# Optimization experiments

Hardware: AMD Instinct MI355X
Metric: run time of the kernel (lower is better)

Reference implementation:

```python
import jax, jax.numpy as jnp
import numpy as np

G = 60            # 60x60 macroblock MV grid (960px / 16px blocks)
IMAGE_SIZE = 960.0
LN_EPS = 1e-5


def layer_norm(x, g, b):
    mu = jnp.mean(x, -1, keepdims=True)
    var = jnp.var(x, -1, keepdims=True)
    return (x - mu) / jnp.sqrt(var + LN_EPS) * g + b


def setup_inputs() -> dict:
    key = jax.random.key(0)
    ks = iter(jax.random.split(key, 40))
    nk = lambda: next(ks)
    N = 4096
    MVF, BED, H = 64, 32, 128
    D_IN = MVF + BED  # 96

    def lin(out_d, in_d):
        w = jax.random.normal(nk(), (out_d, in_d), jnp.float32) * np.float32(1.0 / np.sqrt(in_d))
        b = jnp.zeros((out_d,), jnp.float32)
        return w, b

    motion_vectors = jax.random.normal(nk(), (1, 2, G, G), jnp.float32)
    xy = jax.random.uniform(nk(), (N, 2), jnp.float32, 0.0, 800.0)
    wh = jax.random.uniform(nk(), (N, 2), jnp.float32, 16.0, 160.0)
    boxes = jnp.concatenate([xy, jnp.clip(xy + wh, 0.0, IMAGE_SIZE)], axis=-1)

    inp = {"motion_vectors": motion_vectors, "boxes": boxes}
    # stats projection: 6 stats (mean/std/range x 2 channels) -> MVF
    inp["W_stats"], inp["b_stats"] = lin(MVF, 6)
    inp["g_stats"] = jnp.ones((MVF,), jnp.float32); inp["be_stats"] = jnp.zeros((MVF,), jnp.float32)
    # box coordinate encoder
    inp["W_b1"], inp["b_b1"] = lin(BED, 4)
    inp["g_b1"] = jnp.ones((BED,), jnp.float32); inp["be_b1"] = jnp.zeros((BED,), jnp.float32)
    inp["W_b2"], inp["b_b2"] = lin(BED, BED)
    inp["g_b2"] = jnp.ones((BED,), jnp.float32); inp["be_b2"] = jnp.zeros((BED,), jnp.float32)
    # single-layer LSTM (torch gate order i,f,g,o)
    inp["W_ih"] = jax.random.normal(nk(), (4 * H, D_IN), jnp.float32) * np.float32(1.0 / np.sqrt(D_IN))
    inp["W_hh"] = jax.random.normal(nk(), (4 * H, H), jnp.float32) * np.float32(1.0 / np.sqrt(H))
    inp["b_ih"] = jnp.zeros((4 * H,), jnp.float32)
    inp["b_hh"] = jnp.zeros((4 * H,), jnp.float32)
    # heads
    inp["W_p1"], inp["b_p1"] = lin(H // 2, H); inp["W_p2"], inp["b_p2"] = lin(2, H // 2)
    inp["W_s1"], inp["b_s1"] = lin(H // 2, H); inp["W_s2"], inp["b_s2"] = lin(2, H // 2)
    inp["W_c1"], inp["b_c1"] = lin(H // 2, H); inp["W_c2"], inp["b_c2"] = lin(1, H // 2)
    return inp


def _box_motion_stats(motion_vectors, boxes_norm):
    # motion_vectors: [1,2,G,G]; boxes_norm: [N,4] in [0,1]
    mvf = motion_vectors[0].reshape(2, G * G)  # [2, 3600]
    x1 = jnp.clip(jnp.floor(boxes_norm[:, 0] * G).astype(jnp.int32), 0, G - 1)
    y1 = jnp.clip(jnp.floor(boxes_norm[:, 1] * G).astype(jnp.int32), 0, G - 1)
    x2 = jnp.clip(jnp.ceil(boxes_norm[:, 2] * G).astype(jnp.int32), x1 + 1, G)
    y2 = jnp.clip(jnp.ceil(boxes_norm[:, 3] * G).astype(jnp.int32), y1 + 1, G)
    idx = jnp.arange(G)
    mx = (idx[None, :] >= x1[:, None]) & (idx[None, :] < x2[:, None])  # [N,G]
    my = (idx[None, :] >= y1[:, None]) & (idx[None, :] < y2[:, None])  # [N,G]
    mask = (my[:, :, None] & mx[:, None, :]).reshape(-1, G * G).astype(mvf.dtype)  # [N,3600]
    cnt = mask.sum(-1, keepdims=True)  # >= 1 by construction
    s = jnp.einsum('nc,kc->nk', mask, mvf)          # [N,2]
    sq = jnp.einsum('nc,kc->nk', mask, mvf * mvf)   # [N,2]
    mean = s / cnt
    std = jnp.sqrt(jnp.clip(sq / cnt - mean * mean, 0.0))
    big = jnp.asarray(1e30, mvf.dtype)
    hi = jnp.where(mask[:, None, :] > 0, mvf[None], -big).max(-1)  # [N,2]
    lo = jnp.where(mask[:, None, :] > 0, mvf[None], big).min(-1)   # [N,2]
    return jnp.concatenate([mean, std, hi - lo], axis=-1)  # [N,6]


def reference(motion_vectors, boxes,
              W_stats, b_stats, g_stats, be_stats,
              W_b1, b_b1, g_b1, be_b1, W_b2, b_b2, g_b2, be_b2,
              W_ih, W_hh, b_ih, b_hh,
              W_p1, b_p1, W_p2, b_p2, W_s1, b_s1, W_s2, b_s2, W_c1, b_c1, W_c2, b_c2):
    N = boxes.shape[0]
    H = W_hh.shape[1]
    boxes_norm = jnp.clip(boxes / IMAGE_SIZE, 0.0, 1.0)

    # per-box motion feature (BoxAlignedMotionEncoder: gather region -> mean/std/range -> proj)
    stats = _box_motion_stats(motion_vectors, boxes_norm)
    mv_feat = jax.nn.relu(layer_norm(stats @ W_stats.T + b_stats, g_stats, be_stats))  # [N,64]

    # box coordinate encoder (dropout = identity in eval)
    h1 = jax.nn.relu(layer_norm(boxes_norm @ W_b1.T + b_b1, g_b1, be_b1))
    box_feat = jax.nn.relu(layer_norm(h1 @ W_b2.T + b_b2, g_b2, be_b2))  # [N,32]

    x = jnp.concatenate([mv_feat, box_feat], axis=-1)  # [N,96]

    # single-step LSTM, zero initial state, torch gate order i,f,g,o
    h0 = jnp.zeros((N, H), x.dtype)
    c0 = jnp.zeros((N, H), x.dtype)
    gates = x @ W_ih.T + h0 @ W_hh.T + b_ih + b_hh
    i, f, g, o = jnp.split(gates, 4, axis=-1)
    c = jax.nn.sigmoid(f) * c0 + jax.nn.sigmoid(i) * jnp.tanh(g)
    h = jax.nn.sigmoid(o) * jnp.tanh(c)  # [N,128]

    pos = jax.nn.relu(h @ W_p1.T + b_p1) @ W_p2.T + b_p2    # [N,2]
    size = jax.nn.relu(h @ W_s1.T + b_s1) @ W_s2.T + b_s2   # [N,2]
    conf = jax.nn.relu(h @ W_c1.T + b_c1) @ W_c2.T + b_c2   # [N,1]
    confidences = jax.nn.sigmoid(conf[:, 0])

    # box update: shift center by deltas, scale w/h by exp(size_deltas)
    x1, y1, x2, y2 = boxes[:, 0], boxes[:, 1], boxes[:, 2], boxes[:, 3]
    cx, cy = (x1 + x2) * 0.5, (y1 + y2) * 0.5
    w, hgt = x2 - x1, y2 - y1
    ncx, ncy = cx + pos[:, 0], cy + pos[:, 1]
    nw, nh = w * jnp.exp(size[:, 0]), hgt * jnp.exp(size[:, 1])
    pred = jnp.stack([ncx - nw * 0.5, ncy - nh * 0.5, ncx + nw * 0.5, ncy + nh * 0.5], axis=-1)
    return jnp.concatenate([pred, confidences[:, None]], axis=-1)  # [N,5]
```

## Files before the change

kernel.cpp:

```cpp
#include <hip/hip_runtime.h>
#include <math.h>

#define GRID_G 60
#define GRID_GG 3600
#define BPB 8

__device__ __forceinline__ float wred32sum(float v){
  #pragma unroll
  for (int m = 16; m; m >>= 1) v += __shfl_xor(v, m, 32);
  return v;
}
__device__ __forceinline__ float wred32max(float v){
  #pragma unroll
  for (int m = 16; m; m >>= 1) v = fmaxf(v, __shfl_xor(v, m, 32));
  return v;
}
__device__ __forceinline__ float wred32min(float v){
  #pragma unroll
  for (int m = 16; m; m >>= 1) v = fminf(v, __shfl_xor(v, m, 32));
  return v;
}
__device__ __forceinline__ float frcp(float x){ return __builtin_amdgcn_rcpf(x); }
__device__ __forceinline__ float fsig(float x){ return frcp(1.0f + __expf(-x)); }
__device__ __forceinline__ float ftanh(float x){ return 1.0f - 2.0f * frcp(1.0f + __expf(2.0f * x)); }

__global__ __launch_bounds__(256) void tracker_kernel(
    const float* __restrict__ mv,
    const float* __restrict__ boxes,
    const float* __restrict__ W_stats, const float* __restrict__ b_stats,
    const float* __restrict__ g_stats, const float* __restrict__ be_stats,
    const float* __restrict__ W_b1,  const float* __restrict__ b_b1,
    const float* __restrict__ g_b1,  const float* __restrict__ be_b1,
    const float* __restrict__ W_b2,  const float* __restrict__ b_b2,
    const float* __restrict__ g_b2,  const float* __restrict__ be_b2,
    const float* __restrict__ W_ih,  const float* __restrict__ b_ih,
    const float* __restrict__ b_hh,
    const float* __restrict__ W_p1,  const float* __restrict__ b_p1,
    const float* __restrict__ W_p2,  const float* __restrict__ b_p2,
    const float* __restrict__ W_s1,  const float* __restrict__ b_s1,
    const float* __restrict__ W_s2,  const float* __restrict__ b_s2,
    const float* __restrict__ W_c1,  const float* __restrict__ b_c1,
    const float* __restrict__ W_c2,  const float* __restrict__ b_c2,
    float* __restrict__ out, int N)
{
  __shared__ __align__(16) float x_lds[BPB][96];
  __shared__ __align__(16) float h_lds[BPB][128];
  __shared__ __align__(16) float h1_lds[BPB][32];
  __shared__ float u_lds[3*BPB][65];
  __shared__ float res_lds[BPB][5];

  const int tid  = threadIdx.x;
  const int base = blockIdx.x * BPB;

  {
    const int b   = tid >> 5;
    const int l32 = tid & 31;
    int gb = base + b; if (gb >= N) gb = N - 1;
    const float4 bx = ((const float4*)boxes)[gb];
    const float bn0 = fminf(fmaxf(bx.x * (1.0f/960.0f), 0.f), 1.f);
    const float bn1 = fminf(fmaxf(bx.y * (1.0f/960.0f), 0.f), 1.f);
    const float bn2 = fminf(fmaxf(bx.z * (1.0f/960.0f), 0.f), 1.f);
    const float bn3 = fminf(fmaxf(bx.w * (1.0f/960.0f), 0.f), 1.f);

    int x1 = (int)floorf(bn0 * 60.f); x1 = min(max(x1, 0), 59);
    int y1 = (int)floorf(bn1 * 60.f); y1 = min(max(y1, 0), 59);
    int x2 = (int)ceilf (bn2 * 60.f); x2 = min(max(x2, x1 + 1), 60);
    int y2 = (int)ceilf (bn3 * 60.f); y2 = min(max(y2, y1 + 1), 60);
    const int w = x2 - x1, hh = y2 - y1;
    const int cnt = w * hh;
    const float rw = 1.0f / (float)w;

    float s0=0.f, s1=0.f, q0=0.f, q1=0.f;
    float hi0=-1e30f, hi1=-1e30f, lo0=1e30f, lo1=1e30f;
    for (int c = l32; c < cnt; c += 32) {
      const int yy = (int)(((float)c + 0.5f) * rw);
      const int xx = c - yy * w;
      const int idx = (y1 + yy) * GRID_G + (x1 + xx);
      const float m0 = mv[idx];
      const float m1 = mv[GRID_GG + idx];
      s0 += m0; q0 += m0*m0; hi0 = fmaxf(hi0, m0); lo0 = fminf(lo0, m0);
      s1 += m1; q1 += m1*m1; hi1 = fmaxf(hi1, m1); lo1 = fminf(lo1, m1);
    }
    s0 = wred32sum(s0); q0 = wred32sum(q0); hi0 = wred32max(hi0); lo0 = wred32min(lo0);
    s1 = wred32sum(s1); q1 = wred32sum(q1); hi1 = wred32max(hi1); lo1 = wred32min(lo1);
    const float inv = frcp((float)cnt);
    float st[6];
    st[0] = s0 * inv;
    st[1] = s1 * inv;
    st[2] = sqrtf(fmaxf(q0 * inv - st[0]*st[0], 0.f));
    st[3] = sqrtf(fmaxf(q1 * inv - st[1]*st[1], 0.f));
    st[4] = hi0 - lo0;
    st[5] = hi1 - lo1;

    {
      const float* Wr0 = W_stats + l32 * 6;
      const float* Wr1 = W_stats + (l32 + 32) * 6;
      float v0 = b_stats[l32];
      float v1 = b_stats[l32 + 32];
      #pragma unroll
      for (int k = 0; k < 6; ++k) { v0 += st[k] * Wr0[k]; v1 += st[k] * Wr1[k]; }
      const float mu  = wred32sum(v0 + v1) * (1.0f/64.0f);
      const float var = wred32sum(v0*v0 + v1*v1) * (1.0f/64.0f) - mu*mu;
      const float rs  = rsqrtf(var + 1e-5f);
      x_lds[b][l32     ] = fmaxf((v0 - mu) * rs * g_stats[l32     ] + be_stats[l32     ], 0.f);
      x_lds[b][l32 + 32] = fmaxf((v1 - mu) * rs * g_stats[l32 + 32] + be_stats[l32 + 32], 0.f);
    }

    {
      const float* Wr = W_b1 + l32 * 4;
      const float v = b_b1[l32] + bn0*Wr[0] + bn1*Wr[1] + bn2*Wr[2] + bn3*Wr[3];
      const float mu  = wred32sum(v)   * (1.0f/32.0f);
      const float var = wred32sum(v*v) * (1.0f/32.0f) - mu*mu;
      const float h1v = fmaxf((v - mu) * rsqrtf(var + 1e-5f) * g_b1[l32] + be_b1[l32], 0.f);
      h1_lds[b][l32] = h1v;
    }
    __threadfence_block();

    {
      const float* Wr = W_b2 + l32 * 32;
      float v = b_b2[l32];
      #pragma unroll
      for (int kk = 0; kk < 8; ++kk) {
        const float4 hv = *(const float4*)(&h1_lds[b][kk * 4]);
        const float4 wv = *(const float4*)(&Wr[kk * 4]);
        v = fmaf(wv.x,hv.x, fmaf(wv.y,hv.y, fmaf(wv.z,hv.z, fmaf(wv.w,hv.w, v))));
      }
      const float mu  = wred32sum(v)   * (1.0f/32.0f);
      const float var = wred32sum(v*v) * (1.0f/32.0f) - mu*mu;
      const float y = fmaxf((v - mu) * rsqrtf(var + 1e-5f) * g_b2[l32] + be_b2[l32], 0.f);
      x_lds[b][64 + l32] = y;
    }
  }
  __syncthreads();

  {
    const int j  = tid & 127;
    const int b0 = (tid >> 7) * 4;
    float ai[4] = {0,0,0,0}, ag[4] = {0,0,0,0}, ao[4] = {0,0,0,0};
    const float4* Wi = (const float4*)(W_ih + (size_t)(j      ) * 96);
    const float4* Wg = (const float4*)(W_ih + (size_t)(j + 256) * 96);
    const float4* Wo = (const float4*)(W_ih + (size_t)(j + 384) * 96);
    #pragma unroll 4
    for (int kk = 0; kk < 24; ++kk) {
      const float4 wi = Wi[kk], wg = Wg[kk], wo = Wo[kk];
      #pragma unroll
      for (int b = 0; b < 4; ++b) {
        const float4 xv = *(const float4*)(&x_lds[b0 + b][kk * 4]);
        ai[b] = fmaf(wi.x,xv.x, fmaf(wi.y,xv.y, fmaf(wi.z,xv.z, fmaf(wi.w,xv.w, ai[b]))));
        ag[b] = fmaf(wg.x,xv.x, fmaf(wg.y,xv.y, fmaf(wg.z,xv.z, fmaf(wg.w,xv.w, ag[b]))));
        ao[b] = fmaf(wo.x,xv.x, fmaf(wo.y,xv.y, fmaf(wo.z,xv.z, fmaf(wo.w,xv.w, ao[b]))));
      }
    }
    const float bi = b_ih[j      ] + b_hh[j      ];
    const float bg = b_ih[j + 256] + b_hh[j + 256];
    const float bo = b_ih[j + 384] + b_hh[j + 384];
    #pragma unroll
    for (int b = 0; b < 4; ++b) {
      const float c = fsig(ai[b] + bi) * ftanh(ag[b] + bg);
      h_lds[b0 + b][j] = fsig(ao[b] + bo) * ftanh(c);
    }
  }
  __syncthreads();

  if (tid < 192) {
    const int head = tid >> 6;
    const int l    = tid & 63;
    const float* W1 = (head == 0) ? W_p1 : (head == 1) ? W_s1 : W_c1;
    const float* B1 = (head == 0) ? b_p1 : (head == 1) ? b_s1 : b_c1;
    float acc[BPB] = {0,0,0,0,0,0,0,0};
    const float4* Wr = (const float4*)(W1 + (size_t)l * 128);
    #pragma unroll 4
    for (int kk = 0; kk < 32; ++kk) {
      const float4 w = Wr[kk];
      #pragma unroll
      for (int b = 0; b < BPB; ++b) {
        const float4 hv = *(const float4*)(&h_lds[b][kk * 4]);
        acc[b] = fmaf(w.x,hv.x, fmaf(w.y,hv.y, fmaf(w.z,hv.z, fmaf(w.w,hv.w, acc[b]))));
      }
    }
    const float bias = B1[l];
    #pragma unroll
    for (int b = 0; b < BPB; ++b)
      u_lds[head * BPB + b][l] = fmaxf(acc[b] + bias, 0.f);
  }
  __syncthreads();

  if (tid < BPB * 5) {
    const int b = tid / 5, o = tid % 5;
    const int head = (o < 2) ? 0 : (o < 4) ? 1 : 2;
    const float* W2; float bias;
    if      (o == 0) { W2 = W_p2;      bias = b_p2[0]; }
    else if (o == 1) { W2 = W_p2 + 64; bias = b_p2[1]; }
    else if (o == 2) { W2 = W_s2;      bias = b_s2[0]; }
    else if (o == 3) { W2 = W_s2 + 64; bias = b_s2[1]; }
    else             { W2 = W_c2;      bias = b_c2[0]; }
    const float* ur = u_lds[head * BPB + b];
    float a0 = bias, a1 = 0.f, a2 = 0.f, a3 = 0.f;
    #pragma unroll 4
    for (int k = 0; k < 64; k += 4) {
      a0 = fmaf(ur[k  ], W2[k  ], a0);
      a1 = fmaf(ur[k+1], W2[k+1], a1);
      a2 = fmaf(ur[k+2], W2[k+2], a2);
      a3 = fmaf(ur[k+3], W2[k+3], a3);
    }
    res_lds[b][o] = (a0 + a1) + (a2 + a3);
  }
  __syncthreads();

  if (tid < BPB) {
    const int gb = base + tid;
    if (gb < N) {
      const float4 bx = ((const float4*)boxes)[gb];
      const float cx = (bx.x + bx.z) * 0.5f;
      const float cy = (bx.y + bx.w) * 0.5f;
      const float w  = bx.z - bx.x;
      const float hh = bx.w - bx.y;
      const float ncx = cx + res_lds[tid][0];
      const float ncy = cy + res_lds[tid][1];
      const float nw  = w  * __expf(res_lds[tid][2]);
      const float nh  = hh * __expf(res_lds[tid][3]);
      const float cf  = fsig(res_lds[tid][4]);
      float* op = out + (size_t)gb * 5;
      op[0] = ncx - nw * 0.5f;
      op[1] = ncy - nh * 0.5f;
      op[2] = ncx + nw * 0.5f;
      op[3] = ncy + nh * 0.5f;
      op[4] = cf;
    }
  }
}

extern "C" void kernel_launch(void* const* d_in, const int* in_sizes, int n_in,
                              void* d_out, int out_size, void* d_ws, size_t ws_size,
                              hipStream_t stream) {
  (void)n_in; (void)out_size; (void)d_ws; (void)ws_size;
  const float* mv       = (const float*)d_in[0];
  const float* boxes    = (const float*)d_in[1];
  const float* W_stats  = (const float*)d_in[2];
  const float* b_stats  = (const float*)d_in[3];
  const float* g_stats  = (const float*)d_in[4];
  const float* be_stats = (const float*)d_in[5];
  const float* W_b1     = (const float*)d_in[6];
  const float* b_b1     = (const float*)d_in[7];
  const float* g_b1     = (const float*)d_in[8];
  const float* be_b1    = (const float*)d_in[9];
  const float* W_b2     = (const float*)d_in[10];
  const float* b_b2     = (const float*)d_in[11];
  const float* g_b2     = (const float*)d_in[12];
  const float* be_b2    = (const float*)d_in[13];
  const float* W_ih     = (const float*)d_in[14];
  const float* b_ih     = (const float*)d_in[16];
  const float* b_hh     = (const float*)d_in[17];
  const float* W_p1     = (const float*)d_in[18];
  const float* b_p1     = (const float*)d_in[19];
  const float* W_p2     = (const float*)d_in[20];
  const float* b_p2     = (const float*)d_in[21];
  const float* W_s1     = (const float*)d_in[22];
  const float* b_s1     = (const float*)d_in[23];
  const float* W_s2     = (const float*)d_in[24];
  const float* b_s2     = (const float*)d_in[25];
  const float* W_c1     = (const float*)d_in[26];
  const float* b_c1     = (const float*)d_in[27];
  const float* W_c2     = (const float*)d_in[28];
  const float* b_c2     = (const float*)d_in[29];

  const int N = in_sizes[1] / 4;
  const int grid = (N + BPB - 1) / BPB;
  tracker_kernel<<<grid, 256, 0, stream>>>(
      mv, boxes,
      W_stats, b_stats, g_stats, be_stats,
      W_b1, b_b1, g_b1, be_b1,
      W_b2, b_b2, g_b2, be_b2,
      W_ih, b_ih, b_hh,
      W_p1, b_p1, W_p2, b_p2,
      W_s1, b_s1, W_s2, b_s2,
      W_c1, b_c1, W_c2, b_c2,
      (float*)d_out, N);
}
```

Measured before the change: 151.6 us.

## Restructure tracker kernel to single-wavefront blocks of four boxes with DPP reductions

Switches from 256-thread blocks handling 8 boxes to 64-thread (one wavefront) blocks handling 4 boxes, with 16 lanes per box in the stats stage. Cross-lane reductions now use DPP and ds_swizzle/readlane instead of shfl, the box-encoder hidden vector is broadcast via ds_bpermute instead of LDS, and the head layers plus the final output are computed in registers, removing two barriers and two LDS buffers. In exchange each lane does more work per block and weights are re-read by twice as many blocks, raising total L2 weight traffic.

```diff
diff --git a/kernel.cpp b/kernel.cpp
--- a/kernel.cpp
+++ b/kernel.cpp
@@ -3,28 +3,43 @@
 
 #define GRID_G 60
 #define GRID_GG 3600
-#define BPB 8
-
-__device__ __forceinline__ float wred32sum(float v){
-  #pragma unroll
-  for (int m = 16; m; m >>= 1) v += __shfl_xor(v, m, 32);
+
+__device__ __forceinline__ int   f2i(float x){ return __float_as_int(x); }
+__device__ __forceinline__ float i2f(int x){ return __int_as_float(x); }
+
+template<int CTRL>
+__device__ __forceinline__ float dppmov(float v){
+  return i2f(__builtin_amdgcn_update_dpp(0, f2i(v), CTRL, 0xF, 0xF, true));
+}
+__device__ __forceinline__ float red16sum(float v){
+  v += dppmov<0xB1>(v); v += dppmov<0x4E>(v);
+  v += dppmov<0x124>(v); v += dppmov<0x128>(v);
   return v;
 }
-__device__ __forceinline__ float wred32max(float v){
-  #pragma unroll
-  for (int m = 16; m; m >>= 1) v = fmaxf(v, __shfl_xor(v, m, 32));
+__device__ __forceinline__ float red16max(float v){
+  v = fmaxf(v, dppmov<0xB1>(v));  v = fmaxf(v, dppmov<0x4E>(v));
+  v = fmaxf(v, dppmov<0x124>(v)); v = fmaxf(v, dppmov<0x128>(v));
   return v;
 }
-__device__ __forceinline__ float wred32min(float v){
-  #pragma unroll
-  for (int m = 16; m; m >>= 1) v = fminf(v, __shfl_xor(v, m, 32));
+__device__ __forceinline__ float red16min(float v){
+  v = fminf(v, dppmov<0xB1>(v));  v = fminf(v, dppmov<0x4E>(v));
+  v = fminf(v, dppmov<0x124>(v)); v = fminf(v, dppmov<0x128>(v));
   return v;
+}
+__device__ __forceinline__ float swz_xor16(float v){
+  return i2f(__builtin_amdgcn_ds_swizzle(f2i(v), 0x401F));
+}
+__device__ __forceinline__ float rdl(float v, int l){
+  return i2f(__builtin_amdgcn_readlane(f2i(v), l));
+}
+__device__ __forceinline__ float bperm(int idxbytes, float v){
+  return i2f(__builtin_amdgcn_ds_bpermute(idxbytes, f2i(v)));
 }
 __device__ __forceinline__ float frcp(float x){ return __builtin_amdgcn_rcpf(x); }
 __device__ __forceinline__ float fsig(float x){ return frcp(1.0f + __expf(-x)); }
-__device__ __forceinline__ float ftanh(float x){ return 1.0f - 2.0f * frcp(1.0f + __expf(2.0f * x)); }
-
-__global__ __launch_bounds__(256) void tracker_kernel(
+__device__ __forceinline__ float ftanh(float x){ return 1.0f - 2.0f*frcp(1.0f + __expf(2.0f*x)); }
+
+__global__ __launch_bounds__(64) void tracker_kernel(
     const float* __restrict__ mv,
     const float* __restrict__ boxes,
     const float* __restrict__ W_stats, const float* __restrict__ b_stats,
@@ -43,19 +58,16 @@
     const float* __restrict__ W_c2,  const float* __restrict__ b_c2,
     float* __restrict__ out, int N)
 {
-  __shared__ __align__(16) float x_lds[BPB][96];
-  __shared__ __align__(16) float h_lds[BPB][128];
-  __shared__ __align__(16) float h1_lds[BPB][32];
-  __shared__ float u_lds[3*BPB][65];
-  __shared__ float res_lds[BPB][5];
-
-  const int tid  = threadIdx.x;
-  const int base = blockIdx.x * BPB;
-
-  {
-    const int b   = tid >> 5;
-    const int l32 = tid & 31;
-    int gb = base + b; if (gb >= N) gb = N - 1;
+  __shared__ __align__(16) float x_lds[4][104];
+  __shared__ __align__(16) float h_lds[4][128];
+
+  const int lane = threadIdx.x;
+  const int grp  = lane >> 4;
+  const int l16  = lane & 15;
+  const int base = blockIdx.x * 4;
+
+  {
+    int gb = base + grp; if (gb >= N) gb = N - 1;
     const float4 bx = ((const float4*)boxes)[gb];
     const float bn0 = fminf(fmaxf(bx.x * (1.0f/960.0f), 0.f), 1.f);
     const float bn1 = fminf(fmaxf(bx.y * (1.0f/960.0f), 0.f), 1.f);
@@ -72,7 +84,7 @@
 
     float s0=0.f, s1=0.f, q0=0.f, q1=0.f;
     float hi0=-1e30f, hi1=-1e30f, lo0=1e30f, lo1=1e30f;
-    for (int c = l32; c < cnt; c += 32) {
+    for (int c = l16; c < cnt; c += 16) {
       const int yy = (int)(((float)c + 0.5f) * rw);
       const int xx = c - yy * w;
       const int idx = (y1 + yy) * GRID_G + (x1 + xx);
@@ -81,8 +93,8 @@
       s0 += m0; q0 += m0*m0; hi0 = fmaxf(hi0, m0); lo0 = fminf(lo0, m0);
       s1 += m1; q1 += m1*m1; hi1 = fmaxf(hi1, m1); lo1 = fminf(lo1, m1);
     }
-    s0 = wred32sum(s0); q0 = wred32sum(q0); hi0 = wred32max(hi0); lo0 = wred32min(lo0);
-    s1 = wred32sum(s1); q1 = wred32sum(q1); hi1 = wred32max(hi1); lo1 = wred32min(lo1);
+    s0 = red16sum(s0); q0 = red16sum(q0); hi0 = red16max(hi0); lo0 = red16min(lo0);
+    s1 = red16sum(s1); q1 = red16sum(q1); hi1 = red16max(hi1); lo1 = red16min(lo1);
     const float inv = frcp((float)cnt);
     float st[6];
     st[0] = s0 * inv;
@@ -93,139 +105,201 @@
     st[5] = hi1 - lo1;
 
     {
-      const float* Wr0 = W_stats + l32 * 6;
-      const float* Wr1 = W_stats + (l32 + 32) * 6;
-      float v0 = b_stats[l32];
-      float v1 = b_stats[l32 + 32];
-      #pragma unroll
-      for (int k = 0; k < 6; ++k) { v0 += st[k] * Wr0[k]; v1 += st[k] * Wr1[k]; }
-      const float mu  = wred32sum(v0 + v1) * (1.0f/64.0f);
-      const float var = wred32sum(v0*v0 + v1*v1) * (1.0f/64.0f) - mu*mu;
+      float vm[4], vsum = 0.f, vsq = 0.f;
+      #pragma unroll
+      for (int m = 0; m < 4; ++m) {
+        const int row = l16 + 16*m;
+        const float* Wr = W_stats + row * 6;
+        float v = b_stats[row];
+        #pragma unroll
+        for (int k = 0; k < 6; ++k) v = fmaf(st[k], Wr[k], v);
+        vm[m] = v; vsum += v; vsq = fmaf(v, v, vsq);
+      }
+      const float mu  = red16sum(vsum) * (1.0f/64.0f);
+      const float var = red16sum(vsq)  * (1.0f/64.0f) - mu*mu;
       const float rs  = rsqrtf(var + 1e-5f);
-      x_lds[b][l32     ] = fmaxf((v0 - mu) * rs * g_stats[l32     ] + be_stats[l32     ], 0.f);
-      x_lds[b][l32 + 32] = fmaxf((v1 - mu) * rs * g_stats[l32 + 32] + be_stats[l32 + 32], 0.f);
-    }
-
+      #pragma unroll
+      for (int m = 0; m < 4; ++m) {
+        const int row = l16 + 16*m;
+        x_lds[grp][row] = fmaxf((vm[m]-mu)*rs*g_stats[row] + be_stats[row], 0.f);
+      }
+    }
+
+    float h1a, h1b;
     {
-      const float* Wr = W_b1 + l32 * 4;
-      const float v = b_b1[l32] + bn0*Wr[0] + bn1*Wr[1] + bn2*Wr[2] + bn3*Wr[3];
-      const float mu  = wred32sum(v)   * (1.0f/32.0f);
-      const float var = wred32sum(v*v) * (1.0f/32.0f) - mu*mu;
-      const float h1v = fmaxf((v - mu) * rsqrtf(var + 1e-5f) * g_b1[l32] + be_b1[l32], 0.f);
-      h1_lds[b][l32] = h1v;
-    }
-    __threadfence_block();
+      const float* Wa = W_b1 + l16 * 4;
+      const float* Wb = W_b1 + (l16 + 16) * 4;
+      const float v0 = b_b1[l16]    + bn0*Wa[0] + bn1*Wa[1] + bn2*Wa[2] + bn3*Wa[3];
+      const float v1 = b_b1[l16+16] + bn0*Wb[0] + bn1*Wb[1] + bn2*Wb[2] + bn3*Wb[3];
+      const float mu  = red16sum(v0 + v1) * (1.0f/32.0f);
+      const float var = red16sum(v0*v0 + v1*v1) * (1.0f/32.0f) - mu*mu;
+      const float rs  = rsqrtf(var + 1e-5f);
+      h1a = fmaxf((v0-mu)*rs*g_b1[l16]    + be_b1[l16],    0.f);
+      h1b = fmaxf((v1-mu)*rs*g_b1[l16+16] + be_b1[l16+16], 0.f);
+    }
 
     {
-      const float* Wr = W_b2 + l32 * 32;
-      float v = b_b2[l32];
-      #pragma unroll
-      for (int kk = 0; kk < 8; ++kk) {
-        const float4 hv = *(const float4*)(&h1_lds[b][kk * 4]);
-        const float4 wv = *(const float4*)(&Wr[kk * 4]);
-        v = fmaf(wv.x,hv.x, fmaf(wv.y,hv.y, fmaf(wv.z,hv.z, fmaf(wv.w,hv.w, v))));
-      }
-      const float mu  = wred32sum(v)   * (1.0f/32.0f);
-      const float var = wred32sum(v*v) * (1.0f/32.0f) - mu*mu;
-      const float y = fmaxf((v - mu) * rsqrtf(var + 1e-5f) * g_b2[l32] + be_b2[l32], 0.f);
-      x_lds[b][64 + l32] = y;
+      const int gbyte = (lane & 48) << 2;
+      const float* Wa = W_b2 + l16 * 32;
+      const float* Wb = W_b2 + (l16 + 16) * 32;
+      float u0 = b_b2[l16], u1 = b_b2[l16+16];
+      #pragma unroll
+      for (int k = 0; k < 16; ++k) {
+        const float hk = bperm(gbyte + (k << 2), h1a);
+        u0 = fmaf(Wa[k], hk, u0); u1 = fmaf(Wb[k], hk, u1);
+      }
+      #pragma unroll
+      for (int k = 0; k < 16; ++k) {
+        const float hk = bperm(gbyte + (k << 2), h1b);
+        u0 = fmaf(Wa[16+k], hk, u0); u1 = fmaf(Wb[16+k], hk, u1);
+      }
+      const float mu  = red16sum(u0 + u1) * (1.0f/32.0f);
+      const float var = red16sum(u0*u0 + u1*u1) * (1.0f/32.0f) - mu*mu;
+      const float rs  = rsqrtf(var + 1e-5f);
+      x_lds[grp][64 + l16] = fmaxf((u0-mu)*rs*g_b2[l16]    + be_b2[l16],    0.f);
+      x_lds[grp][80 + l16] = fmaxf((u1-mu)*rs*g_b2[l16+16] + be_b2[l16+16], 0.f);
     }
   }
   __syncthreads();
 
-  {
-    const int j  = tid & 127;
-    const int b0 = (tid >> 7) * 4;
-    float ai[4] = {0,0,0,0}, ag[4] = {0,0,0,0}, ao[4] = {0,0,0,0};
-    const float4* Wi = (const float4*)(W_ih + (size_t)(j      ) * 96);
-    const float4* Wg = (const float4*)(W_ih + (size_t)(j + 256) * 96);
-    const float4* Wo = (const float4*)(W_ih + (size_t)(j + 384) * 96);
-    #pragma unroll 4
+  float hA[4], hB[4];
+  {
+    const float4* Wi0 = (const float4*)(W_ih + (size_t)(lane      ) * 96);
+    const float4* Wi1 = (const float4*)(W_ih + (size_t)(lane +  64) * 96);
+    const float4* Wg0 = (const float4*)(W_ih + (size_t)(lane + 256) * 96);
+    const float4* Wg1 = (const float4*)(W_ih + (size_t)(lane + 320) * 96);
+    const float4* Wo0 = (const float4*)(W_ih + (size_t)(lane + 384) * 96);
+    const float4* Wo1 = (const float4*)(W_ih + (size_t)(lane + 448) * 96);
+    float aI0[4]={0,0,0,0}, aI1[4]={0,0,0,0};
+    float aG0[4]={0,0,0,0}, aG1[4]={0,0,0,0};
+    float aO0[4]={0,0,0,0}, aO1[4]={0,0,0,0};
+    #pragma unroll 2
     for (int kk = 0; kk < 24; ++kk) {
-      const float4 wi = Wi[kk], wg = Wg[kk], wo = Wo[kk];
+      const float4 wi0 = Wi0[kk], wi1 = Wi1[kk];
+      const float4 wg0 = Wg0[kk], wg1 = Wg1[kk];
+      const float4 wo0 = Wo0[kk], wo1 = Wo1[kk];
+      float4 xv[4];
+      #pragma unroll
+      for (int b = 0; b < 4; ++b) xv[b] = *(const float4*)(&x_lds[b][kk*4]);
       #pragma unroll
       for (int b = 0; b < 4; ++b) {
-        const float4 xv = *(const float4*)(&x_lds[b0 + b][kk * 4]);
-        ai[b] = fmaf(wi.x,xv.x, fmaf(wi.y,xv.y, fmaf(wi.z,xv.z, fmaf(wi.w,xv.w, ai[b]))));
-        ag[b] = fmaf(wg.x,xv.x, fmaf(wg.y,xv.y, fmaf(wg.z,xv.z, fmaf(wg.w,xv.w, ag[b]))));
-        ao[b] = fmaf(wo.x,xv.x, fmaf(wo.y,xv.y, fmaf(wo.z,xv.z, fmaf(wo.w,xv.w, ao[b]))));
-      }
-    }
-    const float bi = b_ih[j      ] + b_hh[j      ];
-    const float bg = b_ih[j + 256] + b_hh[j + 256];
-    const float bo = b_ih[j + 384] + b_hh[j + 384];
-    #pragma unroll
-    for (int b = 0; b < 4; ++b) {
-      const float c = fsig(ai[b] + bi) * ftanh(ag[b] + bg);
-      h_lds[b0 + b][j] = fsig(ao[b] + bo) * ftanh(c);
+        const float4 x4 = xv[b];
+        aI0[b] = fmaf(wi0.x,x4.x, fmaf(wi0.y,x4.y, fmaf(wi0.z,x4.z, fmaf(wi0.w,x4.w, aI0[b]))));
+        aI1[b] = fmaf(wi1.x,x4.x, fmaf(wi1.y,x4.y, fmaf(wi1.z,x4.z, fmaf(wi1.w,x4.w, aI1[b]))));
+        aG0[b] = fmaf(wg0.x,x4.x, fmaf(wg0.y,x4.y, fmaf(wg0.z,x4.z, fmaf(wg0.w,x4.w, aG0[b]))));
+        aG1[b] = fmaf(wg1.x,x4.x, fmaf(wg1.y,x4.y, fmaf(wg1.z,x4.z, fmaf(wg1.w,x4.w, aG1[b]))));
+        aO0[b] = fmaf(wo0.x,x4.x, fmaf(wo0.y,x4.y, fmaf(wo0.z,x4.z, fmaf(wo0.w,x4.w, aO0[b]))));
+        aO1[b] = fmaf(wo1.x,x4.x, fmaf(wo1.y,x4.y, fmaf(wo1.z,x4.z, fmaf(wo1.w,x4.w, aO1[b]))));
+      }
+    }
+    const float bI0 = b_ih[lane      ] + b_hh[lane      ];
+    const float bI1 = b_ih[lane +  64] + b_hh[lane +  64];
+    const float bG0 = b_ih[lane + 256] + b_hh[lane + 256];
+    const float bG1 = b_ih[lane + 320] + b_hh[lane + 320];
+    const float bO0 = b_ih[lane + 384] + b_hh[lane + 384];
+    const float bO1 = b_ih[lane + 448] + b_hh[lane + 448];
+    #pragma unroll
+    for (int b = 0; b < 4; ++b) {
+      const float c0 = fsig(aI0[b]+bI0) * ftanh(aG0[b]+bG0);
+      const float c1 = fsig(aI1[b]+bI1) * ftanh(aG1[b]+bG1);
+      hA[b] = fsig(aO0[b]+bO0) * ftanh(c0);
+      hB[b] = fsig(aO1[b]+bO1) * ftanh(c1);
+    }
+    #pragma unroll
+    for (int b = 0; b < 4; ++b) {
+      h_lds[b][lane]      = hA[b];
+      h_lds[b][lane + 64] = hB[b];
     }
   }
   __syncthreads();
 
-  if (tid < 192) {
-    const int head = tid >> 6;
-    const int l    = tid & 63;
-    const float* W1 = (head == 0) ? W_p1 : (head == 1) ? W_s1 : W_c1;
-    const float* B1 = (head == 0) ? b_p1 : (head == 1) ? b_s1 : b_c1;
-    float acc[BPB] = {0,0,0,0,0,0,0,0};
-    const float4* Wr = (const float4*)(W1 + (size_t)l * 128);
-    #pragma unroll 4
+  float up[4], us[4], uc[4];
+  {
+    const float4* Wp = (const float4*)(W_p1 + (size_t)lane * 128);
+    const float4* Ws = (const float4*)(W_s1 + (size_t)lane * 128);
+    const float4* Wc = (const float4*)(W_c1 + (size_t)lane * 128);
+    #pragma unroll
+    for (int b = 0; b < 4; ++b) { up[b]=0.f; us[b]=0.f; uc[b]=0.f; }
+    #pragma unroll 2
     for (int kk = 0; kk < 32; ++kk) {
-      const float4 w = Wr[kk];
-      #pragma unroll
-      for (int b = 0; b < BPB; ++b) {
-        const float4 hv = *(const float4*)(&h_lds[b][kk * 4]);
-        acc[b] = fmaf(w.x,hv.x, fmaf(w.y,hv.y, fmaf(w.z,hv.z, fmaf(w.w,hv.w, acc[b]))));
-      }
-    }
-    const float bias = B1[l];
-    #pragma unroll
-    for (int b = 0; b < BPB; ++b)
-      u_lds[head * BPB + b][l] = fmaxf(acc[b] + bias, 0.f);
-  }
-  __syncthreads();
-
-  if (tid < BPB * 5) {
-    const int b = tid / 5, o = tid % 5;
-    const int head = (o < 2) ? 0 : (o < 4) ? 1 : 2;
-    const float* W2; float bias;
-    if      (o == 0) { W2 = W_p2;      bias = b_p2[0]; }
-    else if (o == 1) { W2 = W_p2 + 64; bias = b_p2[1]; }
-    else if (o == 2) { W2 = W_s2;      bias = b_s2[0]; }
-    else if (o == 3) { W2 = W_s2 + 64; bias = b_s2[1]; }
-    else             { W2 = W_c2;      bias = b_c2[0]; }
-    const float* ur = u_lds[head * BPB + b];
-    float a0 = bias, a1 = 0.f, a2 = 0.f, a3 = 0.f;
-    #pragma unroll 4
-    for (int k = 0; k < 64; k += 4) {
-      a0 = fmaf(ur[k  ], W2[k  ], a0);
-      a1 = fmaf(ur[k+1], W2[k+1], a1);
-      a2 = fmaf(ur[k+2], W2[k+2], a2);
-      a3 = fmaf(ur[k+3], W2[k+3], a3);
-    }
-    res_lds[b][o] = (a0 + a1) + (a2 + a3);
-  }
-  __syncthreads();
-
-  if (tid < BPB) {
-    const int gb = base + tid;
-    if (gb < N) {
-      const float4 bx = ((const float4*)boxes)[gb];
-      const float cx = (bx.x + bx.z) * 0.5f;
-      const float cy = (bx.y + bx.w) * 0.5f;
-      const float w  = bx.z - bx.x;
-      const float hh = bx.w - bx.y;
-      const float ncx = cx + res_lds[tid][0];
-      const float ncy = cy + res_lds[tid][1];
-      const float nw  = w  * __expf(res_lds[tid][2]);
-      const float nh  = hh * __expf(res_lds[tid][3]);
-      const float cf  = fsig(res_lds[tid][4]);
-      float* op = out + (size_t)gb * 5;
-      op[0] = ncx - nw * 0.5f;
-      op[1] = ncy - nh * 0.5f;
-      op[2] = ncx + nw * 0.5f;
-      op[3] = ncy + nh * 0.5f;
-      op[4] = cf;
+      const float4 wp = Wp[kk], ws = Ws[kk], wc = Wc[kk];
+      float4 hv[4];
+      #pragma unroll
+      for (int b = 0; b < 4; ++b) hv[b] = *(const float4*)(&h_lds[b][kk*4]);
+      #pragma unroll
+      for (int b = 0; b < 4; ++b) {
+        const float4 h4 = hv[b];
+        up[b] = fmaf(wp.x,h4.x, fmaf(wp.y,h4.y, fmaf(wp.z,h4.z, fmaf(wp.w,h4.w, up[b]))));
+        us[b] = fmaf(ws.x,h4.x, fmaf(ws.y,h4.y, fmaf(ws.z,h4.z, fmaf(ws.w,h4.w, us[b]))));
+        uc[b] = fmaf(wc.x,h4.x, fmaf(wc.y,h4.y, fmaf(wc.z,h4.z, fmaf(wc.w,h4.w, uc[b]))));
+      }
+    }
+    const float bp = b_p1[lane], bs = b_s1[lane], bc = b_c1[lane];
+    #pragma unroll
+    for (int b = 0; b < 4; ++b) {
+      up[b] = fmaxf(up[b] + bp, 0.f);
+      us[b] = fmaxf(us[b] + bs, 0.f);
+      uc[b] = fmaxf(uc[b] + bc, 0.f);
+    }
+  }
+
+  float res[4][5];
+  {
+    const float w2p0 = W_p2[lane], w2p1 = W_p2[64 + lane];
+    const float w2s0 = W_s2[lane], w2s1 = W_s2[64 + lane];
+    const float w2c0 = W_c2[lane];
+    const float bp0 = b_p2[0], bp1 = b_p2[1];
+    const float bs0 = b_s2[0], bs1 = b_s2[1];
+    const float bc0 = b_c2[0];
+    #pragma unroll
+    for (int b = 0; b < 4; ++b) {
+      float pr0 = w2p0 * up[b];
+      float pr1 = w2p1 * up[b];
+      float pr2 = w2s0 * us[b];
+      float pr3 = w2s1 * us[b];
+      float pr4 = w2c0 * uc[b];
+      float r0 = red16sum(pr0); r0 += swz_xor16(r0);
+      float r1 = red16sum(pr1); r1 += swz_xor16(r1);
+      float r2 = red16sum(pr2); r2 += swz_xor16(r2);
+      float r3 = red16sum(pr3); r3 += swz_xor16(r3);
+      float r4 = red16sum(pr4); r4 += swz_xor16(r4);
+      res[b][0] = rdl(r0,0) + rdl(r0,32) + bp0;
+      res[b][1] = rdl(r1,0) + rdl(r1,32) + bp1;
+      res[b][2] = rdl(r2,0) + rdl(r2,32) + bs0;
+      res[b][3] = rdl(r3,0) + rdl(r3,32) + bs1;
+      res[b][4] = rdl(r4,0) + rdl(r4,32) + bc0;
+    }
+  }
+
+  {
+    float val[4][5];
+    #pragma unroll
+    for (int b = 0; b < 4; ++b) {
+      int gb2 = base + b; if (gb2 >= N) gb2 = N - 1;
+      const float4 bb = ((const float4*)boxes)[gb2];
+      const float cx = (bb.x + bb.z) * 0.5f;
+      const float cy = (bb.y + bb.w) * 0.5f;
+      const float w  = bb.z - bb.x;
+      const float hh = bb.w - bb.y;
+      const float ncx = cx + res[b][0];
+      const float ncy = cy + res[b][1];
+      const float nw  = w  * __expf(res[b][2]);
+      const float nh  = hh * __expf(res[b][3]);
+      val[b][0] = ncx - nw * 0.5f;
+      val[b][1] = ncy - nh * 0.5f;
+      val[b][2] = ncx + nw * 0.5f;
+      val[b][3] = ncy + nh * 0.5f;
+      val[b][4] = fsig(res[b][4]);
+    }
+    float ov = 0.f;
+    #pragma unroll
+    for (int b = 0; b < 4; ++b)
+      #pragma unroll
+      for (int o = 0; o < 5; ++o)
+        ov = (lane == b*5 + o) ? val[b][o] : ov;
+    if (lane < 20) {
+      const int bxi = lane / 5;
+      if (base + bxi < N) out[(size_t)base * 5 + lane] = ov;
     }
   }
 }
@@ -265,8 +339,8 @@
   const float* b_c2     = (const float*)d_in[29];
 
   const int N = in_sizes[1] / 4;
-  const int grid = (N + BPB - 1) / BPB;
-  tracker_kernel<<<grid, 256, 0, stream>>>(
+  const int grid = (N + 3) / 4;
+  tracker_kernel<<<grid, 64, 0, stream>>>(
       mv, boxes,
       W_stats, b_stats, g_stats, be_stats,
       W_b1, b_b1, g_b1, be_b1,
```

Result: slower. 156.4 us (+3.2%).

## Pre-transpose LSTM and head weights for coalesced loads with register tiling

Applied to the files above, without the earlier changes.

Adds a small per-call kernel that transposes the used W_ih gate rows and the three head first-layer weights into a k-major workspace layout. The main kernel's gate and head matmuls then read weights with coalesced float4 loads and compute 4 outputs by 4 or 2 batch rows per thread, staging gate pre-activations in a new LDS buffer. The aim is to replace strided per-row weight reads with contiguous ones and to reuse each weight load across more outputs. In exchange it adds an extra kernel launch and workspace traffic each call, plus an extra LDS stage and barrier, and only 192 threads do the matmuls.

```diff
diff --git a/kernel.cpp b/kernel.cpp
--- a/kernel.cpp
+++ b/kernel.cpp
@@ -22,7 +22,28 @@
 }
 __device__ __forceinline__ float frcp(float x){ return __builtin_amdgcn_rcpf(x); }
 __device__ __forceinline__ float fsig(float x){ return frcp(1.0f + __expf(-x)); }
-__device__ __forceinline__ float ftanh(float x){ return 1.0f - 2.0f * frcp(1.0f + __expf(2.0f * x)); }
+__device__ __forceinline__ float ftanh(float x){ return 1.0f - 2.0f*frcp(1.0f + __expf(2.0f*x)); }
+
+__global__ __launch_bounds__(256) void transpose_kernel(
+    const float* __restrict__ W_ih,
+    const float* __restrict__ W_p1, const float* __restrict__ W_s1,
+    const float* __restrict__ W_c1,
+    float* __restrict__ wt_ih, float* __restrict__ wt_h)
+{
+  const int i = blockIdx.x * 256 + threadIdx.x;
+  if (i < 96*384) {
+    const int k = i / 384, r = i % 384;
+    const int row = (r < 128) ? r : (r + 128);
+    wt_ih[i] = W_ih[row * 96 + k];
+  } else {
+    const int j = i - 96*384;
+    if (j < 128*192) {
+      const int k = j / 192, r = j % 192;
+      const float* W = (r < 64) ? W_p1 : (r < 128) ? W_s1 : W_c1;
+      wt_h[j] = W[(r & 63) * 128 + k];
+    }
+  }
+}
 
 __global__ __launch_bounds__(256) void tracker_kernel(
     const float* __restrict__ mv,
@@ -33,17 +54,16 @@
     const float* __restrict__ g_b1,  const float* __restrict__ be_b1,
     const float* __restrict__ W_b2,  const float* __restrict__ b_b2,
     const float* __restrict__ g_b2,  const float* __restrict__ be_b2,
-    const float* __restrict__ W_ih,  const float* __restrict__ b_ih,
-    const float* __restrict__ b_hh,
-    const float* __restrict__ W_p1,  const float* __restrict__ b_p1,
-    const float* __restrict__ W_p2,  const float* __restrict__ b_p2,
-    const float* __restrict__ W_s1,  const float* __restrict__ b_s1,
-    const float* __restrict__ W_s2,  const float* __restrict__ b_s2,
-    const float* __restrict__ W_c1,  const float* __restrict__ b_c1,
-    const float* __restrict__ W_c2,  const float* __restrict__ b_c2,
+    const float* __restrict__ wt_ih,
+    const float* __restrict__ b_ih,  const float* __restrict__ b_hh,
+    const float* __restrict__ wt_h,
+    const float* __restrict__ b_p1,  const float* __restrict__ W_p2, const float* __restrict__ b_p2,
+    const float* __restrict__ b_s1,  const float* __restrict__ W_s2, const float* __restrict__ b_s2,
+    const float* __restrict__ b_c1,  const float* __restrict__ W_c2, const float* __restrict__ b_c2,
     float* __restrict__ out, int N)
 {
   __shared__ __align__(16) float x_lds[BPB][96];
+  __shared__ __align__(16) float gates_lds[BPB][384];
   __shared__ __align__(16) float h_lds[BPB][128];
   __shared__ __align__(16) float h1_lds[BPB][32];
   __shared__ float u_lds[3*BPB][65];
@@ -95,15 +115,14 @@
     {
       const float* Wr0 = W_stats + l32 * 6;
       const float* Wr1 = W_stats + (l32 + 32) * 6;
-      float v0 = b_stats[l32];
-      float v1 = b_stats[l32 + 32];
-      #pragma unroll
-      for (int k = 0; k < 6; ++k) { v0 += st[k] * Wr0[k]; v1 += st[k] * Wr1[k]; }
+      float v0 = b_stats[l32], v1 = b_stats[l32 + 32];
+      #pragma unroll
+      for (int k = 0; k < 6; ++k) { v0 = fmaf(st[k], Wr0[k], v0); v1 = fmaf(st[k], Wr1[k], v1); }
       const float mu  = wred32sum(v0 + v1) * (1.0f/64.0f);
       const float var = wred32sum(v0*v0 + v1*v1) * (1.0f/64.0f) - mu*mu;
       const float rs  = rsqrtf(var + 1e-5f);
-      x_lds[b][l32     ] = fmaxf((v0 - mu) * rs * g_stats[l32     ] + be_stats[l32     ], 0.f);
-      x_lds[b][l32 + 32] = fmaxf((v1 - mu) * rs * g_stats[l32 + 32] + be_stats[l32 + 32], 0.f);
+      x_lds[b][l32     ] = fmaxf((v0-mu)*rs*g_stats[l32     ] + be_stats[l32     ], 0.f);
+      x_lds[b][l32 + 32] = fmaxf((v1-mu)*rs*g_stats[l32 + 32] + be_stats[l32 + 32], 0.f);
     }
 
     {
@@ -111,8 +130,7 @@
       const float v = b_b1[l32] + bn0*Wr[0] + bn1*Wr[1] + bn2*Wr[2] + bn3*Wr[3];
       const float mu  = wred32sum(v)   * (1.0f/32.0f);
       const float var = wred32sum(v*v) * (1.0f/32.0f) - mu*mu;
-      const float h1v = fmaxf((v - mu) * rsqrtf(var + 1e-5f) * g_b1[l32] + be_b1[l32], 0.f);
-      h1_lds[b][l32] = h1v;
+      h1_lds[b][l32] = fmaxf((v - mu) * rsqrtf(var + 1e-5f) * g_b1[l32] + be_b1[l32], 0.f);
     }
     __threadfence_block();
 
@@ -127,61 +145,100 @@
       }
       const float mu  = wred32sum(v)   * (1.0f/32.0f);
       const float var = wred32sum(v*v) * (1.0f/32.0f) - mu*mu;
-      const float y = fmaxf((v - mu) * rsqrtf(var + 1e-5f) * g_b2[l32] + be_b2[l32], 0.f);
-      x_lds[b][64 + l32] = y;
-    }
+      x_lds[b][64 + l32] = fmaxf((v - mu) * rsqrtf(var + 1e-5f) * g_b2[l32] + be_b2[l32], 0.f);
+    }
+  }
+  __syncthreads();
+
+  if (tid < 192) {
+    const int g = (tid < 96) ? tid : tid - 96;
+    const int s = (tid < 96) ? 0 : 1;
+    const int bs = s * 4;
+    float acc[4][4];
+    #pragma unroll
+    for (int b = 0; b < 4; ++b)
+      #pragma unroll
+      for (int j = 0; j < 4; ++j) acc[b][j] = 0.f;
+    const float4* WT = (const float4*)wt_ih;
+    #pragma unroll 2
+    for (int k4 = 0; k4 < 24; ++k4) {
+      float4 wv[4];
+      #pragma unroll
+      for (int kk = 0; kk < 4; ++kk) wv[kk] = WT[(size_t)(4*k4 + kk) * 96 + g];
+      float4 xv[4];
+      #pragma unroll
+      for (int b = 0; b < 4; ++b) xv[b] = *(const float4*)(&x_lds[bs + b][k4 * 4]);
+      #pragma unroll
+      for (int b = 0; b < 4; ++b) {
+        acc[b][0] = fmaf(wv[0].x, xv[b].x, fmaf(wv[1].x, xv[b].y, fmaf(wv[2].x, xv[b].z, fmaf(wv[3].x, xv[b].w, acc[b][0]))));
+        acc[b][1] = fmaf(wv[0].y, xv[b].x, fmaf(wv[1].y, xv[b].y, fmaf(wv[2].y, xv[b].z, fmaf(wv[3].y, xv[b].w, acc[b][1]))));
+        acc[b][2] = fmaf(wv[0].z, xv[b].x, fmaf(wv[1].z, xv[b].y, fmaf(wv[2].z, xv[b].z, fmaf(wv[3].z, xv[b].w, acc[b][2]))));
+        acc[b][3] = fmaf(wv[0].w, xv[b].x, fmaf(wv[1].w, xv[b].y, fmaf(wv[2].w, xv[b].z, fmaf(wv[3].w, xv[b].w, acc[b][3]))));
+      }
+    }
+    #pragma unroll
+    for (int b = 0; b < 4; ++b)
+      #pragma unroll
+      for (int j = 0; j < 4; ++j)
+        gates_lds[bs + b][4*g + j] = acc[b][j];
   }
   __syncthreads();
 
   {
-    const int j  = tid & 127;
-    const int b0 = (tid >> 7) * 4;
-    float ai[4] = {0,0,0,0}, ag[4] = {0,0,0,0}, ao[4] = {0,0,0,0};
-    const float4* Wi = (const float4*)(W_ih + (size_t)(j      ) * 96);
-    const float4* Wg = (const float4*)(W_ih + (size_t)(j + 256) * 96);
-    const float4* Wo = (const float4*)(W_ih + (size_t)(j + 384) * 96);
-    #pragma unroll 4
-    for (int kk = 0; kk < 24; ++kk) {
-      const float4 wi = Wi[kk], wg = Wg[kk], wo = Wo[kk];
-      #pragma unroll
-      for (int b = 0; b < 4; ++b) {
-        const float4 xv = *(const float4*)(&x_lds[b0 + b][kk * 4]);
-        ai[b] = fmaf(wi.x,xv.x, fmaf(wi.y,xv.y, fmaf(wi.z,xv.z, fmaf(wi.w,xv.w, ai[b]))));
-        ag[b] = fmaf(wg.x,xv.x, fmaf(wg.y,xv.y, fmaf(wg.z,xv.z, fmaf(wg.w,xv.w, ag[b]))));
-        ao[b] = fmaf(wo.x,xv.x, fmaf(wo.y,xv.y, fmaf(wo.z,xv.z, fmaf(wo.w,xv.w, ao[b]))));
-      }
-    }
+    const int j    = tid & 127;
+    const int half = tid >> 7;
     const float bi = b_ih[j      ] + b_hh[j      ];
     const float bg = b_ih[j + 256] + b_hh[j + 256];
     const float bo = b_ih[j + 384] + b_hh[j + 384];
     #pragma unroll
-    for (int b = 0; b < 4; ++b) {
-      const float c = fsig(ai[b] + bi) * ftanh(ag[b] + bg);
-      h_lds[b0 + b][j] = fsig(ao[b] + bo) * ftanh(c);
+    for (int bb = 0; bb < 4; ++bb) {
+      const int b = half * 4 + bb;
+      const float ai = gates_lds[b][j      ] + bi;
+      const float ag = gates_lds[b][128 + j] + bg;
+      const float ao = gates_lds[b][256 + j] + bo;
+      const float c  = fsig(ai) * ftanh(ag);
+      h_lds[b][j] = fsig(ao) * ftanh(c);
     }
   }
   __syncthreads();
 
   if (tid < 192) {
-    const int head = tid >> 6;
-    const int l    = tid & 63;
-    const float* W1 = (head == 0) ? W_p1 : (head == 1) ? W_s1 : W_c1;
+    const int s   = tid / 48;
+    const int g48 = tid - s * 48;
+    const int bs  = s * 2;
+    float acc[2][4];
+    #pragma unroll
+    for (int b = 0; b < 2; ++b)
+      #pragma unroll
+      for (int j = 0; j < 4; ++j) acc[b][j] = 0.f;
+    const float4* WT = (const float4*)wt_h;
+    #pragma unroll 2
+    for (int k4 = 0; k4 < 32; ++k4) {
+      float4 wv[4];
+      #pragma unroll
+      for (int kk = 0; kk < 4; ++kk) wv[kk] = WT[(size_t)(4*k4 + kk) * 48 + g48];
+      float4 hv[2];
+      #pragma unroll
+      for (int b = 0; b < 2; ++b) hv[b] = *(const float4*)(&h_lds[bs + b][k4 * 4]);
+      #pragma unroll
+      for (int b = 0; b < 2; ++b) {
+        acc[b][0] = fmaf(wv[0].x, hv[b].x, fmaf(wv[1].x, hv[b].y, fmaf(wv[2].x, hv[b].z, fmaf(wv[3].x, hv[b].w, acc[b][0]))));
+        acc[b][1] = fmaf(wv[0].y, hv[b].x, fmaf(wv[1].y, hv[b].y, fmaf(wv[2].y, hv[b].z, fmaf(wv[3].y, hv[b].w, acc[b][1]))));
+        acc[b][2] = fmaf(wv[0].z, hv[b].x, fmaf(wv[1].z, hv[b].y, fmaf(wv[2].z, hv[b].z, fmaf(wv[3].z, hv[b].w, acc[b][2]))));
+        acc[b][3] = fmaf(wv[0].w, hv[b].x, fmaf(wv[1].w, hv[b].y, fmaf(wv[2].w, hv[b].z, fmaf(wv[3].w, hv[b].w, acc[b][3]))));
+      }
+    }
+    const int r0   = 4 * g48;
+    const int head = r0 >> 6;
+    const int brow = r0 & 63;
     const float* B1 = (head == 0) ? b_p1 : (head == 1) ? b_s1 : b_c1;
-    float acc[BPB] = {0,0,0,0,0,0,0,0};
-    const float4* Wr = (const float4*)(W1 + (size_t)l * 128);
-    #pragma unroll 4
-    for (int kk = 0; kk < 32; ++kk) {
-      const float4 w = Wr[kk];
-      #pragma unroll
-      for (int b = 0; b < BPB; ++b) {
-        const float4 hv = *(const float4*)(&h_lds[b][kk * 4]);
-        acc[b] = fmaf(w.x,hv.x, fmaf(w.y,hv.y, fmaf(w.z,hv.z, fmaf(w.w,hv.w, acc[b]))));
-      }
-    }
-    const float bias = B1[l];
-    #pragma unroll
-    for (int b = 0; b < BPB; ++b)
-      u_lds[head * BPB + b][l] = fmaxf(acc[b] + bias, 0.f);
+    #pragma unroll
+    for (int j = 0; j < 4; ++j) {
+      const float bias = B1[brow + j];
+      #pragma unroll
+      for (int b = 0; b < 2; ++b)
+        u_lds[head * BPB + bs + b][brow + j] = fmaxf(acc[b][j] + bias, 0.f);
+    }
   }
   __syncthreads();
 
@@ -233,7 +290,7 @@
 extern "C" void kernel_launch(void* const* d_in, const int* in_sizes, int n_in,
                               void* d_out, int out_size, void* d_ws, size_t ws_size,
                               hipStream_t stream) {
-  (void)n_in; (void)out_size; (void)d_ws; (void)ws_size;
+  (void)n_in; (void)out_size; (void)ws_size;
   const float* mv       = (const float*)d_in[0];
   const float* boxes    = (const float*)d_in[1];
   const float* W_stats  = (const float*)d_in[2];
@@ -264,6 +321,11 @@
   const float* W_c2     = (const float*)d_in[28];
   const float* b_c2     = (const float*)d_in[29];
 
+  float* wt_ih = (float*)d_ws;
+  float* wt_h  = wt_ih + 96 * 384;
+
+  transpose_kernel<<<240, 256, 0, stream>>>(W_ih, W_p1, W_s1, W_c1, wt_ih, wt_h);
+
   const int N = in_sizes[1] / 4;
   const int grid = (N + BPB - 1) / BPB;
   tracker_kernel<<<grid, 256, 0, stream>>>(
@@ -271,9 +333,10 @@
       W_stats, b_stats, g_stats, be_stats,
       W_b1, b_b1, g_b1, be_b1,
       W_b2, b_b2, g_b2, be_b2,
-      W_ih, b_ih, b_hh,
-      W_p1, b_p1, W_p2, b_p2,
-      W_s1, b_s1, W_s2, b_s2,
-      W_c1, b_c1, W_c2, b_c2,
+      wt_ih, b_ih, b_hh,
+      wt_h,
+      b_p1, W_p2, b_p2,
+      b_s1, W_s2, b_s2,
+      b_c1, W_c2, b_c2,
       (float*)d_out, N);
 }
```

New measurement: 132.6 us. -12.6%, faster.
